# Performance work log

Hardware: AMD Instinct MI355X
Metric: run time of the kernel (lower is better)

The kernel has to match this reference:

```python
import jax, jax.numpy as jnp
import numpy as np

D_MODEL = 1024
NUM_HEADS = 16
HEAD_DIM = D_MODEL // NUM_HEADS
B, L = 4, 2048


def setup_inputs() -> dict:
    key = jax.random.key(0)
    ks = jax.random.split(key, 10)
    s = 1.0 / np.sqrt(D_MODEL)
    inp = {
        "x": jax.random.normal(ks[0], (B, L, D_MODEL), dtype=jnp.float32),
        "mask": jax.random.randint(ks[1], (1, 1, L, L), 0, 2, dtype=jnp.int32),
        "Wq": jax.random.normal(ks[2], (D_MODEL, D_MODEL), dtype=jnp.float32) * s,
        "bq": jnp.zeros((D_MODEL,), dtype=jnp.float32),
        "Wk": jax.random.normal(ks[3], (D_MODEL, D_MODEL), dtype=jnp.float32) * s,
        "bk": jnp.zeros((D_MODEL,), dtype=jnp.float32),
        "Wv": jax.random.normal(ks[4], (D_MODEL, D_MODEL), dtype=jnp.float32) * s,
        "bv": jnp.zeros((D_MODEL,), dtype=jnp.float32),
        "Wo": jax.random.normal(ks[5], (D_MODEL, D_MODEL), dtype=jnp.float32) * s,
        "bo": jnp.zeros((D_MODEL,), dtype=jnp.float32),
    }
    return inp


def reference(x, mask, Wq, bq, Wk, bk, Wv, bv, Wo, bo):
    b, l, d = x.shape
    # projections (torch Linear: x @ W.T + b)
    q = (x @ Wq.T + bq).reshape(b, l, NUM_HEADS, HEAD_DIM).transpose(0, 2, 1, 3)
    k = (x @ Wk.T + bk).reshape(b, l, NUM_HEADS, HEAD_DIM).transpose(0, 2, 1, 3)
    v = (x @ Wv.T + bv).reshape(b, l, NUM_HEADS, HEAD_DIM).transpose(0, 2, 1, 3)
    scale = 1.0 / np.sqrt(HEAD_DIM).astype(np.float32)
    scores = jnp.einsum("bhqd,bhkd->bhqk", q, k) * scale
    scores = jnp.where(mask == 0, jnp.float32(-1e9), scores)
    attn = jax.nn.softmax(scores, axis=-1)
    out = jnp.einsum("bhqk,bhkd->bhqd", attn, v)
    out = out.transpose(0, 2, 1, 3).reshape(b, l, d)
    return out @ Wo.T + bo
```

## Files before the change

kernel.cpp:

```cpp
#include <hip/hip_runtime.h>
#include <stdint.h>

#define LSEQ 2048
#define DMODEL 1024
#define NHEADS 16
#define HDIM 64
#define NBATCH 4

typedef __attribute__((ext_vector_type(8))) __bf16 bf16x8;
typedef __attribute__((ext_vector_type(4))) __bf16 bf16x4;
typedef __attribute__((ext_vector_type(4))) float f32x4;
typedef __attribute__((ext_vector_type(4))) uint32_t u32x4;
typedef __attribute__((ext_vector_type(4))) uint16_t u16x4;

__device__ inline float fexp2(float x) {
#if __has_builtin(__builtin_amdgcn_exp2f)
    return __builtin_amdgcn_exp2f(x);
#else
    float r; asm("v_exp_f32 %0, %1" : "=v"(r) : "v"(x)); return r;
#endif
}

__device__ inline void gload_lds16(const void* g, const void* l) {
    auto gp = reinterpret_cast<const uint32_t __attribute__((address_space(1)))*>(
        reinterpret_cast<uintptr_t>(g));
    auto lp = reinterpret_cast<uint32_t __attribute__((address_space(3)))*>(
        (uint32_t)(uintptr_t)(l));
    __builtin_amdgcn_global_load_lds(gp, lp, 16, 0, 0);
}

__global__ void cvt_f32_bf16(const float* __restrict__ src, __bf16* __restrict__ dst, int n) {
    int idx = blockIdx.x * blockDim.x + threadIdx.x;
    int stride = gridDim.x * blockDim.x;
    for (int i = idx * 4; i < n; i += stride * 4) {
        float4 f = *(const float4*)(src + i);
        bf16x4 v;
        v[0] = (__bf16)f.x; v[1] = (__bf16)f.y; v[2] = (__bf16)f.z; v[3] = (__bf16)f.w;
        *(bf16x4*)(dst + i) = v;
    }
}

__global__ void cvt_w4(const float* __restrict__ a, const float* __restrict__ b,
                       const float* __restrict__ c, const float* __restrict__ d,
                       __bf16* __restrict__ dst) {
    const int t = blockIdx.x * blockDim.x + threadIdx.x;
    const int i4 = t * 4;
    const int m = i4 >> 20;
    const int off = i4 & ((1 << 20) - 1);
    const float* src = (m == 0) ? a : (m == 1) ? b : (m == 2) ? c : d;
    float4 f = *(const float4*)(src + off);
    bf16x4 v;
    v[0] = (__bf16)f.x; v[1] = (__bf16)f.y; v[2] = (__bf16)f.z; v[3] = (__bf16)f.w;
    *(bf16x4*)(dst + i4) = v;
}

__global__ void pack_bias(const float* __restrict__ bq, const float* __restrict__ bk,
                          const float* __restrict__ bv, float* __restrict__ dst) {
    const int i = blockIdx.x * 256 + threadIdx.x;
    dst[i] = (i < 1024) ? bq[i] : (i < 2048) ? bk[i - 1024] : bv[i - 2048];
}

__global__ void pack_mask(const int* __restrict__ mask, unsigned long long* __restrict__ mbits) {
    const int row = blockIdx.x;
    const int w = threadIdx.x >> 6, lane = threadIdx.x & 63;
    const int* mrow = mask + (size_t)row * LSEQ;
#pragma unroll
    for (int it = 0; it < 8; it++) {
        const int c = it * 256 + w * 64 + lane;
        const unsigned long long b = __ballot(mrow[c] != 0);
        if (lane == 0) mbits[(size_t)row * 32 + it * 4 + w] = b;
    }
}

template <int MODE>
__global__ __launch_bounds__(256) void gemm_bt(const __bf16* __restrict__ A,
                                               const __bf16* __restrict__ Bw,
                                               const float* __restrict__ bias,
                                               void* __restrict__ Cout,
                                               int M, int N, int K, float scale) {
    __shared__ __bf16 As[128 * 32];
    __shared__ __bf16 Bs[128 * 32];

    const int nwg = gridDim.x;
    int bid = blockIdx.x;
    bid = (bid & 7) * (nwg >> 3) + (bid >> 3);

    const int nbn = N >> 7;
    const int bm = (bid / nbn) << 7;
    const int bn = (bid % nbn) << 7;
    const int tid = threadIdx.x;
    const int w = tid >> 6, lane = tid & 63;
    const int l15 = lane & 15, l4 = lane >> 4;
    const int wm = (w >> 1) * 64, wn = (w & 1) * 64;

    f32x4 acc[4][4];
    for (int i = 0; i < 4; i++)
        for (int j = 0; j < 4; j++)
            acc[i][j] = (f32x4){0.f, 0.f, 0.f, 0.f};

    const int fa0 = (w * 2 + 0) * 64 + lane;
    const int fa1 = (w * 2 + 1) * 64 + lane;
    const __bf16* gA0 = A + (size_t)(bm + (fa0 >> 2)) * K + (fa0 & 3) * 8;
    const __bf16* gA1 = A + (size_t)(bm + (fa1 >> 2)) * K + (fa1 & 3) * 8;
    const __bf16* gB0 = Bw + (size_t)(bn + (fa0 >> 2)) * K + (fa0 & 3) * 8;
    const __bf16* gB1 = Bw + (size_t)(bn + (fa1 >> 2)) * K + (fa1 & 3) * 8;
    const __bf16* lA0 = &As[(w * 2 + 0) * 512];
    const __bf16* lA1 = &As[(w * 2 + 1) * 512];
    const __bf16* lB0 = &Bs[(w * 2 + 0) * 512];
    const __bf16* lB1 = &Bs[(w * 2 + 1) * 512];

    for (int kt = 0; kt < K; kt += 32) {
        __syncthreads();
        gload_lds16(gA0 + kt, lA0);
        gload_lds16(gA1 + kt, lA1);
        gload_lds16(gB0 + kt, lB0);
        gload_lds16(gB1 + kt, lB1);
        __syncthreads();

        bf16x8 af[4], bw[4];
        for (int i = 0; i < 4; i++)
            af[i] = *(const bf16x8*)&As[(wm + i * 16 + l15) * 32 + l4 * 8];
        for (int j = 0; j < 4; j++)
            bw[j] = *(const bf16x8*)&Bs[(wn + j * 16 + l15) * 32 + l4 * 8];
        for (int i = 0; i < 4; i++)
            for (int j = 0; j < 4; j++)
                acc[i][j] = __builtin_amdgcn_mfma_f32_16x16x32_bf16(af[i], bw[j], acc[i][j], 0, 0, 0);
    }

    for (int i = 0; i < 4; i++) {
        const int row0 = bm + wm + i * 16 + l4 * 4;
        for (int j = 0; j < 4; j++) {
            const int col = bn + wn + j * 16 + l15;
            const float bv = bias[col];
            if (MODE == 0) {
                __bf16* dst = (__bf16*)Cout;
                const int which = col >> 10;
                const int cr = col & 1023;
                const int h = cr >> 6, d = cr & 63;
                const float scl = (which == 0) ? scale : 1.0f;
                for (int jj = 0; jj < 4; jj++) {
                    const int r = row0 + jj;
                    const int b = r >> 11, l = r & (LSEQ - 1);
                    dst[((size_t)which << 23) +
                        (((size_t)(b * NHEADS + h) * LSEQ + l) << 6) + d] =
                        (__bf16)((acc[i][j][jj] + bv) * scl);
                }
            } else {
                float* dst = (float*)Cout;
                for (int jj = 0; jj < 4; jj++) {
                    const int r = row0 + jj;
                    dst[(size_t)r * N + col] = acc[i][j][jj] + bv;
                }
            }
        }
    }
}

__device__ inline void storeV4(uint32_t (*vt)[32], int kpi, int d0,
                               const u16x4& r0, const u16x4& r1) {
    const uint32_t* a = (const uint32_t*)&r0;
    const uint32_t* b = (const uint32_t*)&r1;
#pragma unroll
    for (int jp = 0; jp < 2; jp++) {
        const uint32_t w0 = __builtin_amdgcn_perm(b[jp], a[jp], 0x05040100u);
        const uint32_t w1 = __builtin_amdgcn_perm(b[jp], a[jp], 0x07060302u);
        const int da = d0 + jp * 2, db = da + 1;
        vt[da][(kpi & 3) | (((kpi >> 2) ^ (da & 7)) << 2)] = w0;
        vt[db][(kpi & 3) | (((kpi >> 2) ^ (db & 7)) << 2)] = w1;
    }
}

__global__ __launch_bounds__(512) void attn_fwd(const __bf16* __restrict__ Q,
                                                const __bf16* __restrict__ Kk,
                                                const __bf16* __restrict__ V,
                                                const unsigned long long* __restrict__ mbits,
                                                __bf16* __restrict__ Oout) {
    const int bh = blockIdx.x & 63;
    const int qt = blockIdx.x >> 6;
    const int tid = threadIdx.x;
    const int w = tid >> 6, lane = tid & 63;
    const int l15 = lane & 15, l4 = lane >> 4, l7 = l15 & 7;

    __shared__ __bf16 Ks[2][64 * 64];
    __shared__ uint32_t Vt32[2][64][32];
    __shared__ __bf16 Ps2[8][16][64];

    const int q0 = qt * 128 + w * 16;
    const __bf16* qbase = Q + ((size_t)bh * LSEQ + q0 + l15) * HDIM + l4 * 8;
    const bf16x8 aq0 = *(const bf16x8*)(qbase);
    const bf16x8 aq1 = *(const bf16x8*)(qbase + 32);

    f32x4 o[4];
    for (int f = 0; f < 4; f++) o[f] = (f32x4){0.f, 0.f, 0.f, 0.f};
    float m_run = -1.0e30f, l_run = 0.f;

    const int ck = tid;
    const int koff = ((ck >> 3) << 7) + ((((ck & 7) ^ ((ck >> 3) & 7))) << 4);
    const char* kp0 = (const char*)(Kk + (size_t)bh * LSEQ * HDIM) + koff;
    const int kdst = tid * 8;

    const int kread0 = l15 * 128 + ((l4 ^ l7) << 4);
    const int kread1 = l15 * 128 + (((4 + l4) ^ l7) << 4);
    const int vread0 = l15 * 32 + ((l4 ^ l7) << 2);
    const int vread1 = l15 * 32 + (((4 + l4) ^ l7) << 2);

    const int kpi = tid & 31;
    const int d0 = (tid >> 5) * 4;
    const __bf16* vp0 = V + (size_t)bh * LSEQ * HDIM + (size_t)(2 * kpi) * HDIM + d0;
    const __bf16* vp1 = vp0 + HDIM;

    char* ps2row = (char*)&Ps2[w][l15][0];
    const int xr = (l15 & 3) << 5;
    const int pw0 = (0 * 32 + l4 * 8) ^ xr;
    const int pw1 = (1 * 32 + l4 * 8) ^ xr;
    const int pw2 = (2 * 32 + l4 * 8) ^ xr;
    const int pw3 = (3 * 32 + l4 * 8) ^ xr;
    const int pr0 = (0 * 64 + l4 * 16) ^ xr;
    const int pr1 = (1 * 64 + l4 * 16) ^ xr;

    const uint2* mptr = (const uint2*)(mbits + (size_t)(q0 + l15) * 32);
    const int sh4 = l4 * 4;

    {
        const u16x4 v0 = *(const u16x4*)(vp0);
        const u16x4 v1 = *(const u16x4*)(vp1);
        vp0 += 64 * HDIM; vp1 += 64 * HDIM;
        gload_lds16(kp0, &Ks[0][kdst]);
        kp0 += 8192;
        storeV4(Vt32[0], kpi, d0, v0, v1);
    }
    __syncthreads();

    int cur = 0;
    const int NT = LSEQ / 64;
    for (int t = 0; t < NT; t++) {
        const int nx = cur ^ 1;
        u16x4 nv0, nv1;
        if (t < NT - 1) {
            nv0 = *(const u16x4*)(vp0);
            nv1 = *(const u16x4*)(vp1);
            vp0 += 64 * HDIM; vp1 += 64 * HDIM;
            gload_lds16(kp0, &Ks[nx][kdst]);
            kp0 += 8192;
        }

        const uint2 mw = mptr[t];
        const uint32_t mlo = mw.x >> sh4;
        const uint32_t mhi = mw.y >> sh4;

        const char* ksb = (const char*)&Ks[cur][0];
        f32x4 sf[4];
        __builtin_amdgcn_s_setprio(1);
#pragma unroll
        for (int f = 0; f < 4; f++) {
            const bf16x8 bk0 = *(const bf16x8*)(ksb + f * 2048 + kread0);
            const bf16x8 bk1 = *(const bf16x8*)(ksb + f * 2048 + kread1);
            f32x4 z = (f32x4){0.f, 0.f, 0.f, 0.f};
            z = __builtin_amdgcn_mfma_f32_16x16x32_bf16(bk0, aq0, z, 0, 0, 0);
            z = __builtin_amdgcn_mfma_f32_16x16x32_bf16(bk1, aq1, z, 0, 0, 0);
            sf[f] = z;
        }
        __builtin_amdgcn_s_setprio(0);

        float vmx;
        {
            float a0 = fmaxf(fmaxf(sf[0][0], sf[0][1]), fmaxf(sf[0][2], sf[0][3]));
            float a1 = fmaxf(fmaxf(sf[1][0], sf[1][1]), fmaxf(sf[1][2], sf[1][3]));
            float a2 = fmaxf(fmaxf(sf[2][0], sf[2][1]), fmaxf(sf[2][2], sf[2][3]));
            float a3 = fmaxf(fmaxf(sf[3][0], sf[3][1]), fmaxf(sf[3][2], sf[3][3]));
            vmx = fmaxf(fmaxf(a0, a1), fmaxf(a2, a3));
            vmx = fmaxf(vmx, __shfl_xor(vmx, 16));
            vmx = fmaxf(vmx, __shfl_xor(vmx, 32));
        }

        if (__any(vmx > m_run + 8.f)) {
            const float mnew = fmaxf(m_run, vmx);
            const float alpha = fexp2(m_run - mnew);
            m_run = mnew;
            l_run *= alpha;
            float aO[4];
#pragma unroll
            for (int jj = 0; jj < 4; jj++) aO[jj] = __shfl(alpha, l4 * 4 + jj);
#pragma unroll
            for (int f = 0; f < 4; f++)
#pragma unroll
                for (int jj = 0; jj < 4; jj++) o[f][jj] *= aO[jj];
        }

        float ps = 0.f;
#pragma unroll
        for (int f = 0; f < 4; f++) {
            const uint32_t mword = (f < 2) ? mlo : mhi;
            const int mb = (f & 1) * 16;
            bf16x4 pk;
#pragma unroll
            for (int jj = 0; jj < 4; jj++) {
                float e = fexp2(sf[f][jj] - m_run);
                e = ((mword >> (mb + jj)) & 1u) ? e : 0.f;
                ps += e;
                pk[jj] = (__bf16)e;
            }
            const int off = (f == 0) ? pw0 : (f == 1) ? pw1 : (f == 2) ? pw2 : pw3;
            *(bf16x4*)(ps2row + off) = pk;
        }
        l_run += ps;

        if (t < NT - 1) storeV4(Vt32[nx], kpi, d0, nv0, nv1);

        __builtin_amdgcn_sched_barrier(0);
        const bf16x8 pa0 = *(const bf16x8*)(ps2row + pr0);
        const bf16x8 pa1 = *(const bf16x8*)(ps2row + pr1);

        const uint32_t* vbase = &Vt32[cur][0][0];
        __builtin_amdgcn_s_setprio(1);
#pragma unroll
        for (int f = 0; f < 4; f++) {
            const bf16x8 bv0 = __builtin_bit_cast(bf16x8, *(const u32x4*)(vbase + f * 512 + vread0));
            const bf16x8 bv1 = __builtin_bit_cast(bf16x8, *(const u32x4*)(vbase + f * 512 + vread1));
            o[f] = __builtin_amdgcn_mfma_f32_16x16x32_bf16(pa0, bv0, o[f], 0, 0, 0);
            o[f] = __builtin_amdgcn_mfma_f32_16x16x32_bf16(pa1, bv1, o[f], 0, 0, 0);
        }
        __builtin_amdgcn_s_setprio(0);

        __syncthreads();
        cur = nx;
    }

    const int b = bh >> 4, h = bh & 15;
    float s = l_run;
    s += __shfl_xor(s, 16);
    s += __shfl_xor(s, 32);
    const float inv = 1.0f / fmaxf(s, 1e-30f);
#pragma unroll
    for (int jj = 0; jj < 4; jj++) {
        const float invj = __shfl(inv, l4 * 4 + jj);
        const int l = q0 + l4 * 4 + jj;
#pragma unroll
        for (int f = 0; f < 4; f++)
            Oout[((size_t)b * LSEQ + l) * DMODEL + h * HDIM + f * 16 + l15] =
                (__bf16)(o[f][jj] * invj);
    }
}

extern "C" void kernel_launch(void* const* d_in, const int* in_sizes, int n_in,
                              void* d_out, int out_size, void* d_ws, size_t ws_size,
                              hipStream_t stream) {
    const float* x  = (const float*)d_in[0];
    const int* mask = (const int*)d_in[1];
    const float* Wq = (const float*)d_in[2];
    const float* bq = (const float*)d_in[3];
    const float* Wk = (const float*)d_in[4];
    const float* bk = (const float*)d_in[5];
    const float* Wv = (const float*)d_in[6];
    const float* bv = (const float*)d_in[7];
    const float* Wo = (const float*)d_in[8];
    const float* bo = (const float*)d_in[9];

    char* ws = (char*)d_ws;
    __bf16* xb  = (__bf16*)(ws);
    __bf16* wqb = (__bf16*)(ws + (16u << 20));
    __bf16* wob = (__bf16*)(ws + (22u << 20));
    __bf16* qb  = (__bf16*)(ws + (24u << 20));
    __bf16* ab  = (__bf16*)(ws + (72u << 20));
    unsigned long long* mb = (unsigned long long*)(ws + (88u << 20));
    float* bqkv = (float*)(ws + (89u << 20));

    const __bf16* kb = qb + ((size_t)1 << 23);
    const __bf16* vb = qb + ((size_t)2 << 23);

    const int M = NBATCH * LSEQ;
    const int N = DMODEL;
    const int K = DMODEL;
    const float cs = 0.18033688011112f;

    cvt_f32_bf16<<<2048, 256, 0, stream>>>(x, xb, M * K);
    cvt_w4<<<4096, 256, 0, stream>>>(Wq, Wk, Wv, Wo, wqb);
    pack_bias<<<12, 256, 0, stream>>>(bq, bk, bv, bqkv);
    pack_mask<<<LSEQ, 256, 0, stream>>>(mask, mb);

    gemm_bt<0><<<(M / 128) * (3 * N / 128), 256, 0, stream>>>(
        xb, wqb, bqkv, (void*)qb, M, 3 * N, K, cs);

    attn_fwd<<<(LSEQ / 128) * 64, 512, 0, stream>>>(qb, kb, vb, mb, ab);

    gemm_bt<1><<<(M / 128) * (N / 128), 256, 0, stream>>>(
        ab, wob, bo, d_out, M, N, K, 1.0f);
}
```

Baseline: 252.1 us.

## Single-buffer V tile, compute softmax row sums via MFMA, add occupancy bound

Drops V double buffering in LDS, so each tile is stored at the start of the iteration and guarded by an extra barrier. Row sums of P are now accumulated with an MFMA against a ones vector instead of scalar adds plus final shuffles. Masking uses a bitfield-extract AND instead of a select, and launch_bounds now requests a minimum of 8 blocks. This aims to cut LDS footprint and VALU work and raise occupancy, at the cost of an extra __syncthreads per tile, less overlap of V stores, possible register spills, and row sums taken from bf16-rounded P.

```diff
diff --git a/kernel.cpp b/kernel.cpp
--- a/kernel.cpp
+++ b/kernel.cpp
@@ -18,6 +18,14 @@
     return __builtin_amdgcn_exp2f(x);
 #else
     float r; asm("v_exp_f32 %0, %1" : "=v"(r) : "v"(x)); return r;
+#endif
+}
+
+__device__ inline uint32_t bitmask1(uint32_t m, int pos) {
+#if __has_builtin(__builtin_amdgcn_sbfe)
+    return (uint32_t)__builtin_amdgcn_sbfe((int)m, pos, 1);
+#else
+    return (uint32_t)(((int32_t)(m << (31 - pos))) >> 31);
 #endif
 }
 
@@ -170,11 +178,11 @@
     }
 }
 
-__global__ __launch_bounds__(512) void attn_fwd(const __bf16* __restrict__ Q,
-                                                const __bf16* __restrict__ Kk,
-                                                const __bf16* __restrict__ V,
-                                                const unsigned long long* __restrict__ mbits,
-                                                __bf16* __restrict__ Oout) {
+__global__ __launch_bounds__(512, 8) void attn_fwd(const __bf16* __restrict__ Q,
+                                                   const __bf16* __restrict__ Kk,
+                                                   const __bf16* __restrict__ V,
+                                                   const unsigned long long* __restrict__ mbits,
+                                                   __bf16* __restrict__ Oout) {
     const int bh = blockIdx.x & 63;
     const int qt = blockIdx.x >> 6;
     const int tid = threadIdx.x;
@@ -182,7 +190,7 @@
     const int l15 = lane & 15, l4 = lane >> 4, l7 = l15 & 7;
 
     __shared__ __bf16 Ks[2][64 * 64];
-    __shared__ uint32_t Vt32[2][64][32];
+    __shared__ uint32_t Vt32[64][32];
     __shared__ __bf16 Ps2[8][16][64];
 
     const int q0 = qt * 128 + w * 16;
@@ -190,9 +198,13 @@
     const bf16x8 aq0 = *(const bf16x8*)(qbase);
     const bf16x8 aq1 = *(const bf16x8*)(qbase + 32);
 
+    const u32x4 onesu = {0x3F803F80u, 0x3F803F80u, 0x3F803F80u, 0x3F803F80u};
+    const bf16x8 ones = __builtin_bit_cast(bf16x8, onesu);
+
     f32x4 o[4];
     for (int f = 0; f < 4; f++) o[f] = (f32x4){0.f, 0.f, 0.f, 0.f};
-    float m_run = -1.0e30f, l_run = 0.f;
+    f32x4 lacc = (f32x4){0.f, 0.f, 0.f, 0.f};
+    float m_run = -1.0e30f;
 
     const int ck = tid;
     const int koff = ((ck >> 3) << 7) + ((((ck & 7) ^ ((ck >> 3) & 7))) << 4);
@@ -221,20 +233,20 @@
     const uint2* mptr = (const uint2*)(mbits + (size_t)(q0 + l15) * 32);
     const int sh4 = l4 * 4;
 
-    {
-        const u16x4 v0 = *(const u16x4*)(vp0);
-        const u16x4 v1 = *(const u16x4*)(vp1);
-        vp0 += 64 * HDIM; vp1 += 64 * HDIM;
-        gload_lds16(kp0, &Ks[0][kdst]);
-        kp0 += 8192;
-        storeV4(Vt32[0], kpi, d0, v0, v1);
-    }
+    u16x4 cv0 = *(const u16x4*)(vp0);
+    u16x4 cv1 = *(const u16x4*)(vp1);
+    vp0 += 64 * HDIM; vp1 += 64 * HDIM;
+    gload_lds16(kp0, &Ks[0][kdst]);
+    kp0 += 8192;
     __syncthreads();
 
     int cur = 0;
     const int NT = LSEQ / 64;
     for (int t = 0; t < NT; t++) {
         const int nx = cur ^ 1;
+
+        storeV4(Vt32, kpi, d0, cv0, cv1);
+
         u16x4 nv0, nv1;
         if (t < NT - 1) {
             nv0 = *(const u16x4*)(vp0);
@@ -264,11 +276,12 @@
 
         float vmx;
         {
-            float a0 = fmaxf(fmaxf(sf[0][0], sf[0][1]), fmaxf(sf[0][2], sf[0][3]));
-            float a1 = fmaxf(fmaxf(sf[1][0], sf[1][1]), fmaxf(sf[1][2], sf[1][3]));
-            float a2 = fmaxf(fmaxf(sf[2][0], sf[2][1]), fmaxf(sf[2][2], sf[2][3]));
-            float a3 = fmaxf(fmaxf(sf[3][0], sf[3][1]), fmaxf(sf[3][2], sf[3][3]));
-            vmx = fmaxf(fmaxf(a0, a1), fmaxf(a2, a3));
+            const float t0 = fmaxf(fmaxf(sf[0][0], sf[0][1]), sf[0][2]);
+            const float t1 = fmaxf(fmaxf(sf[0][3], sf[1][0]), sf[1][1]);
+            const float t2 = fmaxf(fmaxf(sf[1][2], sf[1][3]), sf[2][0]);
+            const float t3 = fmaxf(fmaxf(sf[2][1], sf[2][2]), sf[2][3]);
+            const float t4 = fmaxf(fmaxf(sf[3][0], sf[3][1]), sf[3][2]);
+            vmx = fmaxf(fmaxf(fmaxf(t0, t1), t2), fmaxf(fmaxf(t3, t4), sf[3][3]));
             vmx = fmaxf(vmx, __shfl_xor(vmx, 16));
             vmx = fmaxf(vmx, __shfl_xor(vmx, 32));
         }
@@ -277,41 +290,42 @@
             const float mnew = fmaxf(m_run, vmx);
             const float alpha = fexp2(m_run - mnew);
             m_run = mnew;
-            l_run *= alpha;
             float aO[4];
 #pragma unroll
             for (int jj = 0; jj < 4; jj++) aO[jj] = __shfl(alpha, l4 * 4 + jj);
 #pragma unroll
+            for (int jj = 0; jj < 4; jj++) lacc[jj] *= aO[jj];
+#pragma unroll
             for (int f = 0; f < 4; f++)
 #pragma unroll
                 for (int jj = 0; jj < 4; jj++) o[f][jj] *= aO[jj];
         }
 
-        float ps = 0.f;
 #pragma unroll
         for (int f = 0; f < 4; f++) {
             const uint32_t mword = (f < 2) ? mlo : mhi;
-            const int mb = (f & 1) * 16;
+            const int base = (f & 1) * 16;
             bf16x4 pk;
 #pragma unroll
             for (int jj = 0; jj < 4; jj++) {
                 float e = fexp2(sf[f][jj] - m_run);
-                e = ((mword >> (mb + jj)) & 1u) ? e : 0.f;
-                ps += e;
+                const uint32_t msk = bitmask1(mword, base + jj);
+                e = __builtin_bit_cast(float, __builtin_bit_cast(uint32_t, e) & msk);
                 pk[jj] = (__bf16)e;
             }
             const int off = (f == 0) ? pw0 : (f == 1) ? pw1 : (f == 2) ? pw2 : pw3;
             *(bf16x4*)(ps2row + off) = pk;
         }
-        l_run += ps;
-
-        if (t < NT - 1) storeV4(Vt32[nx], kpi, d0, nv0, nv1);
-
-        __builtin_amdgcn_sched_barrier(0);
+
+        __syncthreads();
+
         const bf16x8 pa0 = *(const bf16x8*)(ps2row + pr0);
         const bf16x8 pa1 = *(const bf16x8*)(ps2row + pr1);
 
-        const uint32_t* vbase = &Vt32[cur][0][0];
+        lacc = __builtin_amdgcn_mfma_f32_16x16x32_bf16(pa0, ones, lacc, 0, 0, 0);
+        lacc = __builtin_amdgcn_mfma_f32_16x16x32_bf16(pa1, ones, lacc, 0, 0, 0);
+
+        const uint32_t* vbase = &Vt32[0][0];
         __builtin_amdgcn_s_setprio(1);
 #pragma unroll
         for (int f = 0; f < 4; f++) {
@@ -323,17 +337,14 @@
         __builtin_amdgcn_s_setprio(0);
 
         __syncthreads();
+        cv0 = nv0; cv1 = nv1;
         cur = nx;
     }
 
     const int b = bh >> 4, h = bh & 15;
-    float s = l_run;
-    s += __shfl_xor(s, 16);
-    s += __shfl_xor(s, 32);
-    const float inv = 1.0f / fmaxf(s, 1e-30f);
 #pragma unroll
     for (int jj = 0; jj < 4; jj++) {
-        const float invj = __shfl(inv, l4 * 4 + jj);
+        const float invj = 1.0f / fmaxf(lacc[jj], 1e-30f);
         const int l = q0 + l4 * 4 + jj;
 #pragma unroll
         for (int f = 0; f < 4; f++)
```

Result: slower. 341.0 us (+35.2%).
